# Optimization experiments

Measured on AMD Instinct MI355X. Metric: run time of the kernel, lower is better.

Reference implementation:

```python
import jax, jax.numpy as jnp
import numpy as np

B, S, M, D, H = 2, 2048, 512, 1024, 16
HD = D // H      # head dim 64
KVC = D // 16    # MLA kv compression dim 64
QC = D // 32     # MLA q compression dim 32
RD = HD          # retrieval (qk) head dim 64
LOOKBACK = 8     # cross_window
EPS = 1e-6


def rmsnorm(x, w):
    return x * jax.lax.rsqrt(jnp.mean(x * x, axis=-1, keepdims=True) + EPS) * w


def setup_inputs():
    key = jax.random.key(0)
    ks = jax.random.split(key, 20)
    g = lambda i, shape: jax.random.normal(ks[i], shape, jnp.float32) * 0.02
    return {
        "x": jax.random.normal(ks[0], (B, S, D), jnp.float32),
        "memory": jax.random.normal(ks[1], (B, M, D), jnp.float32),
        "seg_ids": jnp.sort(jax.random.randint(ks[2], (B, S), 0, M), axis=-1),
        "norm1_w": jnp.ones((D,), jnp.float32),
        "W_dq": g(3, (D, QC)),
        "W_uq": g(4, (QC, H * RD)),
        "W_dkv": g(5, (D, KVC)),
        "W_uk": g(6, (KVC, H * RD)),
        "W_uv": g(7, (KVC, H * HD)),
        "W_o_self": g(8, (H * HD, D)),
        "norm2_w": jnp.ones((D,), jnp.float32),
        "W_q_c": g(9, (D, D)),
        "W_k_c": g(10, (D, D)),
        "W_v_c": g(11, (D, D)),
        "W_o_c": g(12, (D, D)),
        "norm3_w": jnp.ones((D,), jnp.float32),
        "W_gate": g(13, (D, 4 * D)),
        "W_up": g(14, (D, 4 * D)),
        "W_down": g(15, (4 * D, D)),
    }


def reference(x, memory, seg_ids, norm1_w, W_dq, W_uq, W_dkv, W_uk, W_uv,
              W_o_self, norm2_w, W_q_c, W_k_c, W_v_c, W_o_c, norm3_w,
              W_gate, W_up, W_down):
    # ---- MLA causal self-attention (low-rank compressed q/kv) ----
    h = rmsnorm(x, norm1_w)
    q = ((h @ W_dq) @ W_uq).reshape(B, S, H, RD)
    c_kv = h @ W_dkv                                  # [B,S,KVC]
    k = (c_kv @ W_uk).reshape(B, S, H, RD)
    v = (c_kv @ W_uv).reshape(B, S, H, HD)
    scores = jnp.einsum('bihd,bjhd->bhij', q, k) / np.float32(np.sqrt(RD))
    causal = jnp.tril(jnp.ones((S, S), bool))
    scores = jnp.where(causal, scores, -jnp.inf)
    attn = jax.nn.softmax(scores, axis=-1)
    o = jnp.einsum('bhij,bjhd->bihd', attn, v).reshape(B, S, H * HD)
    x = x + o @ W_o_self
    # ---- segment sliding-window cross-attention ----
    h = rmsnorm(x, norm2_w)
    qc = (h @ W_q_c).reshape(B, S, H, HD)
    kc = (memory @ W_k_c).reshape(B, M, H, HD)
    vc = (memory @ W_v_c).reshape(B, M, H, HD)
    sc = jnp.einsum('bihd,bjhd->bhij', qc, kc) / np.float32(np.sqrt(HD))
    kv_pos = jnp.arange(M)
    seg = seg_ids[:, :, None]                          # [B,S,1]
    allowed = (kv_pos[None, None, :] <= seg) & (kv_pos[None, None, :] >= seg - LOOKBACK)
    sc = jnp.where(allowed[:, None, :, :], sc, -jnp.inf)
    ac = jax.nn.softmax(sc, axis=-1)
    oc = jnp.einsum('bhij,bjhd->bihd', ac, vc).reshape(B, S, D)
    x = x + oc @ W_o_c
    # ---- SwiGLU FFN ----
    h = rmsnorm(x, norm3_w)
    x = x + (jax.nn.silu(h @ W_gate) * (h @ W_up)) @ W_down
    return x
```

## Files before the change

### kernel.cpp

```cpp
#include <hip/hip_runtime.h>
#include <stdint.h>

typedef unsigned short U16;
typedef __bf16 bf16x8 __attribute__((ext_vector_type(8)));
typedef unsigned short us8 __attribute__((ext_vector_type(8)));
typedef float f32x4 __attribute__((ext_vector_type(4)));

__device__ __forceinline__ U16 f2bf(float f) {
    unsigned u = __builtin_bit_cast(unsigned, f);
    unsigned r = (u + 0x7fff + ((u >> 16) & 1)) >> 16;
    return (U16)r;
}
__device__ __forceinline__ U16 f2bf_fast(float f) {
    return (U16)((__builtin_bit_cast(unsigned, f) + 0x8000u) >> 16);
}
__device__ __forceinline__ float bf2f(U16 v) {
    return __builtin_bit_cast(float, (unsigned)v << 16);
}
__device__ __forceinline__ bf16x8 ld8(const U16* p) { return __builtin_bit_cast(bf16x8, *(const us8*)p); }

__device__ __forceinline__ void async16(const U16* g, U16* l) {
    auto* gp = (const __attribute__((address_space(1))) U16*)g;
    auto* lp = (__attribute__((address_space(3))) U16*)(uintptr_t)(uint32_t)(uintptr_t)l;
    __builtin_amdgcn_global_load_lds(gp, lp, 16, 0, 0);
}

struct WEnt { const float* src; U16* dst; int K, N, Kpad, Npad, koff, noff, tiles; };
struct WTable { WEnt e[13]; };

__global__ __launch_bounds__(256) void wtrans_all(WTable t) {
    int bx = blockIdx.x, ei = 0;
    while (bx >= t.e[ei].tiles) { bx -= t.e[ei].tiles; ei++; }
    const WEnt E = t.e[ei];
    const int ntn = E.Npad >> 5;
    const int n0 = (bx % ntn) * 32, k0 = (bx / ntn) * 32;
    __shared__ float tile[32][33];
    const int tx = threadIdx.x & 31, ty = threadIdx.x >> 5;
#pragma unroll
    for (int i = 0; i < 4; i++) {
        int kk = k0 + ty + i * 8, n = n0 + tx;
        int k = kk - E.koff;
        float v = (k >= 0 && k < E.K && n < E.N) ? E.src[(size_t)k * E.N + n] : 0.f;
        tile[ty + i * 8][tx] = v;
    }
    __syncthreads();
#pragma unroll
    for (int i = 0; i < 4; i++) {
        int n = n0 + ty + i * 8, kk = k0 + tx;
        E.dst[(size_t)(E.noff + n) * E.Kpad + kk] = f2bf(tile[tx][ty + i * 8]);
    }
}

__global__ __launch_bounds__(256) void f2bf_k(const float* __restrict__ in, U16* __restrict__ out, int n) {
    int i = (blockIdx.x * 256 + threadIdx.x) * 4;
    if (i < n) {
        float4 v = *(const float4*)(in + i);
        out[i + 0] = f2bf(v.x); out[i + 1] = f2bf(v.y);
        out[i + 2] = f2bf(v.z); out[i + 3] = f2bf(v.w);
    }
}

__global__ __launch_bounds__(256) void cq_reduce(const float* __restrict__ p, U16* __restrict__ out) {
    int i = (blockIdx.x * 256 + threadIdx.x) * 4;
    const float4 a = *(const float4*)(p + i);
    const float4 b = *(const float4*)(p + 524288 + i);
    const float4 c = *(const float4*)(p + 2 * 524288 + i);
    const float4 d = *(const float4*)(p + 3 * 524288 + i);
    out[i + 0] = f2bf(a.x + b.x + c.x + d.x);
    out[i + 1] = f2bf(a.y + b.y + c.y + d.y);
    out[i + 2] = f2bf(a.z + b.z + c.z + d.z);
    out[i + 3] = f2bf(a.w + b.w + c.w + d.w);
}

__global__ __launch_bounds__(256) void rmsnorm_k(const float* __restrict__ x, const float* __restrict__ w,
                                                 U16* __restrict__ h) {
    const int row = blockIdx.x, tid = threadIdx.x;
    const float4 v = *(const float4*)(x + (size_t)row * 1024 + tid * 4);
    float ss = v.x * v.x + v.y * v.y + v.z * v.z + v.w * v.w;
#pragma unroll
    for (int o = 32; o > 0; o >>= 1) ss += __shfl_xor(ss, o);
    __shared__ float red[4];
    if ((tid & 63) == 0) red[tid >> 6] = ss;
    __syncthreads();
    float tot = red[0] + red[1] + red[2] + red[3];
    float sc = rsqrtf(tot * (1.0f / 1024.0f) + 1e-6f);
    const float4 wv = *(const float4*)(w + tid * 4);
    U16* hp = h + (size_t)row * 1024 + tid * 4;
    hp[0] = f2bf(v.x * sc * wv.x); hp[1] = f2bf(v.y * sc * wv.y);
    hp[2] = f2bf(v.z * sc * wv.z); hp[3] = f2bf(v.w * sc * wv.w);
}

__global__ __launch_bounds__(256) void qkuv_gemm(const U16* __restrict__ A, const U16* __restrict__ Wuqk,
                                                 const U16* __restrict__ Wuv,
                                                 U16* __restrict__ qkb, U16* __restrict__ vt) {
    __shared__ __align__(16) U16 As[2][128 * 32];
    __shared__ __align__(16) U16 Bs[2][128 * 32];
    __shared__ __align__(16) U16 Ts[4][64 * 80];
    const int tid = threadIdx.x;
    const bool isuv = blockIdx.x >= 16;
    const U16* Bt = isuv ? Wuv : Wuqk;
    const int n0 = (isuv ? blockIdx.x - 16 : blockIdx.x) * 128;
    const int m0 = blockIdx.y * 128;
    const int wave = tid >> 6, lane = tid & 63, l16 = lane & 15, quad = lane >> 4;
    const int wm = (wave >> 1) * 64, wn = (wave & 1) * 64;
    const int sr = lane >> 2, sc = (lane & 3) * 8;
    const U16* gA = A + (size_t)(m0 + wave * 32 + sr) * 128 + sc;
    const U16* gB = Bt + (size_t)(n0 + wave * 32 + sr) * 128 + sc;
    f32x4 acc[4][4] = {};
    for (int kt = 0; kt < 128; kt += 64) {
        __syncthreads();
#pragma unroll
        for (int p = 0; p < 2; p++) {
            const int o = kt + p * 32;
            async16(gA + o, &As[p][(wave * 32) * 32]);
            async16(gA + 16 * 128 + o, &As[p][(wave * 32 + 16) * 32]);
            async16(gB + o, &Bs[p][(wave * 32) * 32]);
            async16(gB + 16 * 128 + o, &Bs[p][(wave * 32 + 16) * 32]);
        }
        __syncthreads();
#pragma unroll
        for (int p = 0; p < 2; p++) {
            bf16x8 af[4], bfr[4];
#pragma unroll
            for (int i = 0; i < 4; i++) {
                af[i]  = ld8(&As[p][(wm + i * 16 + l16) * 32 + quad * 8]);
                bfr[i] = ld8(&Bs[p][(wn + i * 16 + l16) * 32 + quad * 8]);
            }
#pragma unroll
            for (int mi = 0; mi < 4; mi++)
#pragma unroll
                for (int ni = 0; ni < 4; ni++)
                    acc[mi][ni] = __builtin_amdgcn_mfma_f32_16x16x32_bf16(af[mi], bfr[ni], acc[mi][ni], 0, 0, 0);
        }
    }
    if (isuv) {
        U16* T = Ts[wave];
#pragma unroll
        for (int mi = 0; mi < 4; mi++)
#pragma unroll
            for (int ni = 0; ni < 4; ni++)
#pragma unroll
                for (int r = 0; r < 4; r++)
                    T[(ni * 16 + l16) * 80 + mi * 16 + quad * 4 + r] = f2bf(acc[mi][ni][r]);
#pragma unroll
        for (int c = 0; c < 8; c++) {
            int nloc = (lane >> 3) + 8 * c, mloc = (lane & 7) * 8;
            us8 v = *(const us8*)&T[nloc * 80 + mloc];
            *(us8*)&vt[(size_t)(n0 + wn + nloc) * 4096 + (m0 + wm + mloc)] = v;
        }
    } else {
#pragma unroll
        for (int mi = 0; mi < 4; mi++)
#pragma unroll
            for (int r = 0; r < 4; r++) {
                int m = m0 + wm + mi * 16 + quad * 4 + r;
#pragma unroll
                for (int ni = 0; ni < 4; ni++)
                    qkb[(size_t)m * 2048 + n0 + wn + ni * 16 + l16] = f2bf(acc[mi][ni][r]);
            }
    }
}

template <int EPI>
__global__ __launch_bounds__(256) void gemm_m64(const U16* __restrict__ A, const U16* __restrict__ Bt,
                                                void* __restrict__ Cout, const float* __restrict__ resid,
                                                int M, int N, int K, int lda, int ldb, int ldc) {
    __shared__ __align__(16) U16 As[2][2][64 * 32];
    __shared__ __align__(16) U16 Bs[2][2][128 * 32];
    const int tid = threadIdx.x;
    const int m0 = blockIdx.y * 64, n0 = blockIdx.x * 128;
    const int k0 = blockIdx.z * K;
    const int wave = tid >> 6, lane = tid & 63, l16 = lane & 15, quad = lane >> 4;
    const int wm = (wave >> 1) * 32, wn = (wave & 1) * 64;
    const int sr = lane >> 2, sc = (lane & 3) * 8;
    const U16* gA = A + (size_t)(m0 + wave * 16 + sr) * lda + sc + k0;
    const U16* gB = Bt + (size_t)(n0 + wave * 32 + sr) * ldb + sc + k0;

    auto STAGE = [&](int buf, int kt) {
#pragma unroll
        for (int p = 0; p < 2; p++) {
            const int o = kt + p * 32;
            async16(gA + o, &As[buf][p][(wave * 16) * 32]);
            async16(gB + o, &Bs[buf][p][(wave * 32) * 32]);
            async16(gB + (size_t)16 * ldb + o, &Bs[buf][p][(wave * 32 + 16) * 32]);
        }
    };

    f32x4 acc[2][4] = {};
    const int NTK = K >> 6;
    STAGE(0, 0);
    STAGE(1, 64);
#pragma unroll 1
    for (int t = 0; t < NTK; ++t) {
        if (t == NTK - 1) asm volatile("s_waitcnt vmcnt(0)" ::: "memory");
        else              asm volatile("s_waitcnt vmcnt(6)" ::: "memory");
        __builtin_amdgcn_s_barrier();
        __builtin_amdgcn_sched_barrier(0);
        const int buf = t & 1;
#pragma unroll
        for (int p = 0; p < 2; p++) {
            bf16x8 af[2], bfr[4];
#pragma unroll
            for (int i = 0; i < 2; i++)
                af[i] = ld8(&As[buf][p][(wm + i * 16 + l16) * 32 + quad * 8]);
#pragma unroll
            for (int i = 0; i < 4; i++)
                bfr[i] = ld8(&Bs[buf][p][(wn + i * 16 + l16) * 32 + quad * 8]);
#pragma unroll
            for (int mi = 0; mi < 2; mi++)
#pragma unroll
                for (int ni = 0; ni < 4; ni++)
                    acc[mi][ni] = __builtin_amdgcn_mfma_f32_16x16x32_bf16(af[mi], bfr[ni], acc[mi][ni], 0, 0, 0);
        }
        __builtin_amdgcn_s_barrier();
        if (t + 2 < NTK) STAGE(buf, (t + 2) * 64);
    }
#pragma unroll
    for (int mi = 0; mi < 2; mi++) {
#pragma unroll
        for (int r = 0; r < 4; r++) {
            int m = m0 + wm + mi * 16 + quad * 4 + r;
#pragma unroll
            for (int ni = 0; ni < 4; ni++) {
                int n = n0 + wn + ni * 16 + l16;
                float val = acc[mi][ni][r];
                if (EPI == 0) ((U16*)Cout)[(size_t)m * ldc + n] = f2bf(val);
                else if (EPI == 1) ((float*)Cout)[(size_t)m * ldc + n] = resid[(size_t)m * ldc + n] + val;
                else if (EPI == 5) ((float*)Cout)[(size_t)blockIdx.z * 524288 + (size_t)m * ldc + n] = val;
            }
        }
    }
}

__global__ __launch_bounds__(256) void qckv_gemm(const U16* __restrict__ hbuf, const U16* __restrict__ Wqc,
                                                 const U16* __restrict__ memb, const U16* __restrict__ Wkvc,
                                                 U16* __restrict__ qcb, U16* __restrict__ kvcb) {
    __shared__ __align__(16) U16 As[2][2][64 * 32];
    __shared__ __align__(16) U16 Bs[2][2][128 * 32];
    const int tid = threadIdx.x, bid = blockIdx.x;
    const U16 *A, *Bt; U16* C; int m0, n0, ldc;
    if (bid < 512) { A = hbuf; Bt = Wqc;  C = qcb;  m0 = (bid >> 3) * 64; n0 = (bid & 7) * 128;  ldc = 1024; }
    else { int b2 = bid - 512; A = memb; Bt = Wkvc; C = kvcb; m0 = (b2 >> 4) * 64; n0 = (b2 & 15) * 128; ldc = 2048; }
    const int wave = tid >> 6, lane = tid & 63, l16 = lane & 15, quad = lane >> 4;
    const int wm = (wave >> 1) * 32, wn = (wave & 1) * 64;
    const int sr = lane >> 2, sc = (lane & 3) * 8;
    const U16* gA = A + (size_t)(m0 + wave * 16 + sr) * 1024 + sc;
    const U16* gB = Bt + (size_t)(n0 + wave * 32 + sr) * 1024 + sc;

    auto STAGE = [&](int buf, int kt) {
#pragma unroll
        for (int p = 0; p < 2; p++) {
            const int o = kt + p * 32;
            async16(gA + o, &As[buf][p][(wave * 16) * 32]);
            async16(gB + o, &Bs[buf][p][(wave * 32) * 32]);
            async16(gB + 16 * 1024 + o, &Bs[buf][p][(wave * 32 + 16) * 32]);
        }
    };

    f32x4 acc[2][4] = {};
    STAGE(0, 0);
    STAGE(1, 64);
#pragma unroll 1
    for (int t = 0; t < 16; ++t) {
        if (t == 15) asm volatile("s_waitcnt vmcnt(0)" ::: "memory");
        else         asm volatile("s_waitcnt vmcnt(6)" ::: "memory");
        __builtin_amdgcn_s_barrier();
        __builtin_amdgcn_sched_barrier(0);
        const int buf = t & 1;
#pragma unroll
        for (int p = 0; p < 2; p++) {
            bf16x8 af[2], bfr[4];
#pragma unroll
            for (int i = 0; i < 2; i++)
                af[i] = ld8(&As[buf][p][(wm + i * 16 + l16) * 32 + quad * 8]);
#pragma unroll
            for (int i = 0; i < 4; i++)
                bfr[i] = ld8(&Bs[buf][p][(wn + i * 16 + l16) * 32 + quad * 8]);
#pragma unroll
            for (int mi = 0; mi < 2; mi++)
#pragma unroll
                for (int ni = 0; ni < 4; ni++)
                    acc[mi][ni] = __builtin_amdgcn_mfma_f32_16x16x32_bf16(af[mi], bfr[ni], acc[mi][ni], 0, 0, 0);
        }
        __builtin_amdgcn_s_barrier();
        if (t + 2 < 16) STAGE(buf, (t + 2) * 64);
    }
#pragma unroll
    for (int mi = 0; mi < 2; mi++)
#pragma unroll
        for (int r = 0; r < 4; r++) {
            int m = m0 + wm + mi * 16 + quad * 4 + r;
#pragma unroll
            for (int ni = 0; ni < 4; ni++)
                C[(size_t)m * ldc + n0 + wn + ni * 16 + l16] = f2bf(acc[mi][ni][r]);
        }
}

__global__ __launch_bounds__(512, 2) void ffn1_8ph(const U16* __restrict__ A, const U16* __restrict__ Wgu,
                                                   U16* __restrict__ Cout) {
    __shared__ __align__(16) U16 As[2][256 * 64];
    __shared__ __align__(16) U16 Bs[2][256 * 64];
    const int tid = threadIdx.x;
    const int wid = tid >> 6, lane = tid & 63;
    const int l16 = lane & 15, quad = lane >> 4;
    const int n0 = blockIdx.x * 128;
    const int m0 = blockIdx.y * 256;
    const int wr = wid >> 2, wc = wid & 3;
    const int wm = wr * 128;
    const int wn = wc * 64;
    const int srow = lane >> 3;
    const int schunk = (lane & 7) ^ srow;
    const U16* gA = A + (size_t)(m0 + wid * 32 + srow) * 1024 + schunk * 8;
    const U16* gB = Wgu + (size_t)((wid & 1) * 4096 + n0 + (wid >> 1) * 32 + srow) * 1024 + schunk * 8;

    auto STAGE = [&](int buf, int kt) {
        U16* la = &As[buf][(wid * 32) * 64];
        U16* lb = &Bs[buf][(wid * 32) * 64];
        const U16* pa = gA + kt;
        const U16* pb = gB + kt;
#pragma unroll
        for (int j = 0; j < 4; ++j) {
            async16(pa + j * 8 * 1024, la + j * 8 * 64);
            async16(pb + j * 8 * 1024, lb + j * 8 * 64);
        }
    };

    f32x4 acc[8][4] = {};

    auto TILE = [&](int buf) {
        const U16* Ab = &As[buf][0];
        const U16* Bb = &Bs[buf][0];
        const int cx = l16 & 7;
        bf16x8 a0[4][2], a1[4][2], b0[2][2], b1[2][2];
#pragma unroll
        for (int mi = 0; mi < 4; ++mi)
#pragma unroll
            for (int kh = 0; kh < 2; ++kh)
                a0[mi][kh] = ld8(&Ab[(wm + mi * 16 + l16) * 64 + (((kh * 4 + quad) ^ cx) << 3)]);
#pragma unroll
        for (int ni = 0; ni < 2; ++ni)
#pragma unroll
            for (int kh = 0; kh < 2; ++kh)
                b0[ni][kh] = ld8(&Bb[(wn + ni * 16 + l16) * 64 + (((kh * 4 + quad) ^ cx) << 3)]);
#pragma unroll
        for (int ni = 0; ni < 2; ++ni)
#pragma unroll
            for (int kh = 0; kh < 2; ++kh)
                b1[ni][kh] = ld8(&Bb[(wn + 32 + ni * 16 + l16) * 64 + (((kh * 4 + quad) ^ cx) << 3)]);
        __builtin_amdgcn_s_setprio(1);
#pragma unroll
        for (int mi = 0; mi < 4; ++mi)
#pragma unroll
            for (int ni = 0; ni < 2; ++ni)
#pragma unroll
                for (int kh = 0; kh < 2; ++kh)
                    acc[mi][ni] = __builtin_amdgcn_mfma_f32_16x16x32_bf16(a0[mi][kh], b0[ni][kh], acc[mi][ni], 0, 0, 0);
        __builtin_amdgcn_s_setprio(0);
#pragma unroll
        for (int mi = 0; mi < 4; ++mi)
#pragma unroll
            for (int kh = 0; kh < 2; ++kh)
                a1[mi][kh] = ld8(&Ab[(wm + 64 + mi * 16 + l16) * 64 + (((kh * 4 + quad) ^ cx) << 3)]);
        __builtin_amdgcn_s_setprio(1);
#pragma unroll
        for (int mi = 0; mi < 4; ++mi)
#pragma unroll
            for (int ni = 0; ni < 2; ++ni)
#pragma unroll
                for (int kh = 0; kh < 2; ++kh)
                    acc[mi][2 + ni] = __builtin_amdgcn_mfma_f32_16x16x32_bf16(a0[mi][kh], b1[ni][kh], acc[mi][2 + ni], 0, 0, 0);
        __builtin_amdgcn_s_setprio(0);
        __builtin_amdgcn_s_setprio(1);
#pragma unroll
        for (int mi = 0; mi < 4; ++mi)
#pragma unroll
            for (int ni = 0; ni < 2; ++ni)
#pragma unroll
                for (int kh = 0; kh < 2; ++kh)
                    acc[4 + mi][2 + ni] = __builtin_amdgcn_mfma_f32_16x16x32_bf16(a1[mi][kh], b1[ni][kh], acc[4 + mi][2 + ni], 0, 0, 0);
        __builtin_amdgcn_s_setprio(0);
        __builtin_amdgcn_s_setprio(1);
#pragma unroll
        for (int mi = 0; mi < 4; ++mi)
#pragma unroll
            for (int ni = 0; ni < 2; ++ni)
#pragma unroll
                for (int kh = 0; kh < 2; ++kh)
                    acc[4 + mi][ni] = __builtin_amdgcn_mfma_f32_16x16x32_bf16(a1[mi][kh], b0[ni][kh], acc[4 + mi][ni], 0, 0, 0);
        __builtin_amdgcn_s_setprio(0);
    };

    STAGE(0, 0);
    STAGE(1, 64);
#pragma unroll 1
    for (int t2 = 0; t2 < 7; ++t2) {
        asm volatile("s_waitcnt vmcnt(8)" ::: "memory");
        __builtin_amdgcn_s_barrier();
        __builtin_amdgcn_sched_barrier(0);
        TILE(0);
        __builtin_amdgcn_s_barrier();
        STAGE(0, (2 * t2 + 2) * 64);
        asm volatile("s_waitcnt vmcnt(8)" ::: "memory");
        __builtin_amdgcn_s_barrier();
        __builtin_amdgcn_sched_barrier(0);
        TILE(1);
        __builtin_amdgcn_s_barrier();
        STAGE(1, (2 * t2 + 3) * 64);
    }
    asm volatile("s_waitcnt vmcnt(8)" ::: "memory");
    __builtin_amdgcn_s_barrier();
    __builtin_amdgcn_sched_barrier(0);
    TILE(0);
    asm volatile("s_waitcnt vmcnt(0)" ::: "memory");
    __builtin_amdgcn_s_barrier();
    __builtin_amdgcn_sched_barrier(0);
    TILE(1);

#pragma unroll
    for (int mi = 0; mi < 8; ++mi)
#pragma unroll
        for (int r = 0; r < 4; ++r) {
            int m = m0 + wm + mi * 16 + quad * 4 + r;
#pragma unroll
            for (int ni = 0; ni < 2; ++ni) {
                int col = n0 + wc * 32 + ni * 16 + l16;
                float g = acc[mi][ni][r], u = acc[mi][ni + 2][r];
                float act = g / (1.f + __expf(-g)) * u;
                Cout[(size_t)m * 4096 + col] = f2bf(act);
            }
        }
}

__global__ __launch_bounds__(256, 3) void flash_self4(const U16* __restrict__ QK, const U16* __restrict__ Vt,
                                                      U16* __restrict__ Og) {
    __shared__ __align__(16) U16 Ks[2][32 * 64];
    __shared__ __align__(16) U16 Vs[2][64 * 32];
    __shared__ __align__(16) U16 Ps[4][1280];
    const int wave = threadIdx.x >> 6, lane = threadIdx.x & 63;
    const int l16 = lane & 15, quad = lane >> 4;
    const int bx = blockIdx.x;
    const int T = 15 - (bx >> 5);
    const int bh = bx & 31, b = bh >> 4, h = bh & 15;
    const int q0 = T * 128;
    const int NT = 4 * T + 4;
    const int G0 = q0 + wave * 16, G1 = q0 + 64 + wave * 16;
    bf16x8 aq[2][2];
    {
        const size_t r0 = (size_t)(b * 2048 + G0 + l16) * 2048 + h * 64;
        const size_t r1 = (size_t)(b * 2048 + G1 + l16) * 2048 + h * 64;
        aq[0][0] = ld8(QK + r0 + quad * 8); aq[0][1] = ld8(QK + r0 + 32 + quad * 8);
        aq[1][0] = ld8(QK + r1 + quad * 8); aq[1][1] = ld8(QK + r1 + 32 + quad * 8);
    }
    const int krow = wave * 8 + (lane >> 3);
    const int kchunk = (lane & 7) ^ (lane >> 3);
    const U16* gK = QK + (size_t)(b * 2048 + krow) * 2048 + 1024 + h * 64 + kchunk * 8;
    const int vrow = wave * 16 + (lane >> 2);
    const int vchunk = (lane & 3) ^ ((lane >> 2) & 3) ^ ((lane >> 4) & 3);
    const U16* gV = Vt + (size_t)(h * 64 + vrow) * 4096 + b * 2048 + vchunk * 8;

    auto STAGE = [&](int buf, int j0) {
        async16(gK + (size_t)j0 * 2048, &Ks[buf][(wave * 8) * 64]);
        async16(gV + j0, &Vs[buf][(wave * 16) * 32]);
    };

    f32x4 o[2][4] = {};
    float ls[2][4] = {};
    U16* Pw = Ps[wave];
    const int prd = l16 * 40 + ((quad ^ (l16 >> 2)) << 3);

    auto TILE = [&](int buf, int j0) {
        bf16x8 kf[2][2];
#pragma unroll
        for (int jh = 0; jh < 2; ++jh)
#pragma unroll
            for (int kh = 0; kh < 2; ++kh)
                kf[jh][kh] = ld8(&Ks[buf][(jh * 16 + l16) * 64 + (((kh * 4 + quad) ^ (l16 & 7)) << 3)]);
        bf16x8 vf[4];
#pragma unroll
        for (int dg = 0; dg < 4; ++dg)
            vf[dg] = ld8(&Vs[buf][(dg * 16 + l16) * 32 + ((quad ^ (l16 & 3) ^ ((l16 >> 2) & 3)) << 3)]);
#pragma unroll
        for (int g = 0; g < 2; ++g) {
            const int G = g ? G1 : G0;
            if (j0 < G + 16) {
                f32x4 s0 = {}, s1 = {};
                __builtin_amdgcn_s_setprio(1);
                s0 = __builtin_amdgcn_mfma_f32_16x16x32_bf16(aq[g][0], kf[0][0], s0, 0, 0, 0);
                s0 = __builtin_amdgcn_mfma_f32_16x16x32_bf16(aq[g][1], kf[0][1], s0, 0, 0, 0);
                s1 = __builtin_amdgcn_mfma_f32_16x16x32_bf16(aq[g][0], kf[1][0], s1, 0, 0, 0);
                s1 = __builtin_amdgcn_mfma_f32_16x16x32_bf16(aq[g][1], kf[1][1], s1, 0, 0, 0);
                __builtin_amdgcn_s_setprio(0);
                float p0[4], p1[4];
                if (j0 + 32 > G) {
#pragma unroll
                    for (int r = 0; r < 4; ++r) {
                        int qg = G + quad * 4 + r;
                        p0[r] = (j0 + l16 <= qg) ? __expf(fminf(s0[r] * 0.125f, 30.f)) : 0.f;
                        p1[r] = (j0 + 16 + l16 <= qg) ? __expf(fminf(s1[r] * 0.125f, 30.f)) : 0.f;
                    }
                } else {
#pragma unroll
                    for (int r = 0; r < 4; ++r) {
                        p0[r] = __expf(fminf(s0[r] * 0.125f, 30.f));
                        p1[r] = __expf(fminf(s1[r] * 0.125f, 30.f));
                    }
                }
#pragma unroll
                for (int r = 0; r < 4; ++r) {
                    ls[g][r] += p0[r] + p1[r];
                    int row = quad * 4 + r;
                    Pw[g * 640 + row * 40 + ((((l16 >> 3) + 0) ^ quad) << 3) + (l16 & 7)] = f2bf_fast(p0[r]);
                    Pw[g * 640 + row * 40 + ((((l16 >> 3) + 2) ^ quad) << 3) + (l16 & 7)] = f2bf_fast(p1[r]);
                }
                bf16x8 ap = ld8(&Pw[g * 640 + prd]);
                __builtin_amdgcn_s_setprio(1);
                o[g][0] = __builtin_amdgcn_mfma_f32_16x16x32_bf16(ap, vf[0], o[g][0], 0, 0, 0);
                o[g][1] = __builtin_amdgcn_mfma_f32_16x16x32_bf16(ap, vf[1], o[g][1], 0, 0, 0);
                o[g][2] = __builtin_amdgcn_mfma_f32_16x16x32_bf16(ap, vf[2], o[g][2], 0, 0, 0);
                o[g][3] = __builtin_amdgcn_mfma_f32_16x16x32_bf16(ap, vf[3], o[g][3], 0, 0, 0);
                __builtin_amdgcn_s_setprio(0);
            }
        }
    };

    STAGE(0, 0);
    STAGE(1, 32);
#pragma unroll 1
    for (int it = 0; it < NT - 2; ++it) {
        asm volatile("s_waitcnt vmcnt(2)" ::: "memory");
        __builtin_amdgcn_s_barrier();
        __builtin_amdgcn_sched_barrier(0);
        TILE(it & 1, it * 32);
        __builtin_amdgcn_s_barrier();
        STAGE(it & 1, (it + 2) * 32);
    }
    asm volatile("s_waitcnt vmcnt(2)" ::: "memory");
    __builtin_amdgcn_s_barrier();
    __builtin_amdgcn_sched_barrier(0);
    TILE(NT & 1, (NT - 2) * 32);
    asm volatile("s_waitcnt vmcnt(0)" ::: "memory");
    __builtin_amdgcn_s_barrier();
    __builtin_amdgcn_sched_barrier(0);
    TILE((NT - 1) & 1, (NT - 1) * 32);

#pragma unroll
    for (int g = 0; g < 2; ++g) {
        const int G = g ? G1 : G0;
#pragma unroll
        for (int r = 0; r < 4; ++r) {
            float v = ls[g][r];
            v += __shfl_xor(v, 1); v += __shfl_xor(v, 2);
            v += __shfl_xor(v, 4); v += __shfl_xor(v, 8);
            float inv = 1.0f / v;
            int qrow = G + quad * 4 + r;
            U16* op = Og + (size_t)(b * 2048 + qrow) * 1024 + h * 64 + l16;
#pragma unroll
            for (int dg = 0; dg < 4; ++dg)
                op[dg * 16] = f2bf(o[g][dg][r] * inv);
        }
    }
}

__global__ __launch_bounds__(256) void cross_attn(const U16* __restrict__ qc, const U16* __restrict__ kvc,
                                                  const int* __restrict__ seg_ids, U16* __restrict__ oc) {
    const int tok = blockIdx.x;
    const int b = tok >> 11;
    const int w = threadIdx.x >> 6, lane = threadIdx.x & 63;
    const int h = blockIdx.y * 4 + w;
    const int seg = seg_ids[tok];
    const size_t qoff = (size_t)tok * 1024 + h * 64 + lane;
    float q = bf2f(qc[qoff]);
    float s[9];
#pragma unroll
    for (int jj = 0; jj < 9; jj++) {
        int j = seg - 8 + jj;
        float sc = -INFINITY;
        if (j >= 0) {
            float kv = bf2f(kvc[((size_t)(b * 512) + j) * 2048 + h * 64 + lane]);
            sc = q * kv;
            sc += __shfl_xor(sc, 1); sc += __shfl_xor(sc, 2); sc += __shfl_xor(sc, 4);
            sc += __shfl_xor(sc, 8); sc += __shfl_xor(sc, 16); sc += __shfl_xor(sc, 32);
            sc *= 0.125f;
        }
        s[jj] = sc;
    }
    float m = s[0];
#pragma unroll
    for (int jj = 1; jj < 9; jj++) m = fmaxf(m, s[jj]);
    float l = 0.f, o = 0.f;
#pragma unroll
    for (int jj = 0; jj < 9; jj++) {
        int j = seg - 8 + jj;
        if (j >= 0) {
            float p = __expf(s[jj] - m);
            l += p;
            o += p * bf2f(kvc[((size_t)(b * 512) + j) * 2048 + 1024 + h * 64 + lane]);
        }
    }
    oc[qoff] = f2bf(o / l);
}

extern "C" void kernel_launch(void* const* d_in, const int* in_sizes, int n_in,
                              void* d_out, int out_size, void* d_ws, size_t ws_size,
                              hipStream_t stream) {
    const float* x      = (const float*)d_in[0];
    const float* memory = (const float*)d_in[1];
    const int*   seg    = (const int*)d_in[2];
    const float* n1w    = (const float*)d_in[3];
    const float* W_dq   = (const float*)d_in[4];
    const float* W_uq   = (const float*)d_in[5];
    const float* W_dkv  = (const float*)d_in[6];
    const float* W_uk   = (const float*)d_in[7];
    const float* W_uv   = (const float*)d_in[8];
    const float* W_os   = (const float*)d_in[9];
    const float* n2w    = (const float*)d_in[10];
    const float* W_qc   = (const float*)d_in[11];
    const float* W_kc   = (const float*)d_in[12];
    const float* W_vc   = (const float*)d_in[13];
    const float* W_oc   = (const float*)d_in[14];
    const float* n3w    = (const float*)d_in[15];
    const float* W_gate = (const float*)d_in[16];
    const float* W_up   = (const float*)d_in[17];
    const float* W_down = (const float*)d_in[18];
    (void)in_sizes; (void)n_in; (void)out_size; (void)ws_size;

    char* ws = (char*)d_ws;
    size_t off = 0;
    auto alloc = [&](size_t bytes) -> void* {
        void* p = ws + off;
        off += (bytes + 255) & ~(size_t)255;
        return p;
    };
    const size_t MB = 1024 * 1024;
    U16* hbuf     = (U16*)alloc(8 * MB);
    float* x1     = (float*)alloc(16 * MB);
    float* x2     = (float*)alloc(16 * MB);
    float* cq32   = (float*)alloc(8 * MB);
    U16* Wt_dqkv  = (U16*)alloc(128 * 1024 * 2);
    U16* Wt_uqk   = (U16*)alloc(2048 * 128 * 2);
    U16* Wt_uv    = (U16*)alloc(1024 * 128 * 2);
    U16* Wt_os    = (U16*)alloc(1024 * 1024 * 2);
    U16* Wt_qc    = (U16*)alloc(1024 * 1024 * 2);
    U16* Wt_kvc   = (U16*)alloc((size_t)2048 * 1024 * 2);
    U16* Wt_oc    = (U16*)alloc(1024 * 1024 * 2);
    U16* Wt_gu    = (U16*)alloc((size_t)8192 * 1024 * 2);
    U16* Wt_down  = (U16*)alloc((size_t)1024 * 4096 * 2);
    U16* mem_bf   = (U16*)alloc(1024 * 1024 * 2);
    char* arena   = ws + off;
    U16* cq  = (U16*)(arena);
    U16* qkb = (U16*)(arena + 1 * MB);
    U16* vt  = (U16*)(arena + 17 * MB);
    U16* ob  = (U16*)(arena + 25 * MB);
    U16* qcb  = (U16*)(arena);
    U16* kvcb = (U16*)(arena + 8 * MB);
    U16* ocb  = (U16*)(arena + 12 * MB);
    U16* gact = (U16*)(arena);

    WTable T;
    int i = 0;
    auto ent = [&](const float* s, U16* d, int K, int N, int Kpad, int Npad, int koff, int noff) {
        T.e[i++] = WEnt{s, d, K, N, Kpad, Npad, koff, noff, (Kpad >> 5) * (Npad >> 5)};
    };
    ent(W_dq,   Wt_dqkv, 1024, 32,   1024, 32,   0,  0);
    ent(W_dkv,  Wt_dqkv, 1024, 64,   1024, 96,   0,  32);
    ent(W_uq,   Wt_uqk,  32,   1024, 128,  1024, 0,  0);
    ent(W_uk,   Wt_uqk,  64,   1024, 128,  1024, 32, 1024);
    ent(W_uv,   Wt_uv,   64,   1024, 128,  1024, 32, 0);
    ent(W_os,   Wt_os,   1024, 1024, 1024, 1024, 0,  0);
    ent(W_qc,   Wt_qc,   1024, 1024, 1024, 1024, 0,  0);
    ent(W_kc,   Wt_kvc,  1024, 1024, 1024, 1024, 0,  0);
    ent(W_vc,   Wt_kvc,  1024, 1024, 1024, 1024, 0,  1024);
    ent(W_oc,   Wt_oc,   1024, 1024, 1024, 1024, 0,  0);
    ent(W_gate, Wt_gu,   1024, 4096, 1024, 4096, 0,  0);
    ent(W_up,   Wt_gu,   1024, 4096, 1024, 4096, 0,  4096);
    ent(W_down, Wt_down, 4096, 1024, 4096, 1024, 0,  0);
    int total_tiles = 0;
    for (int j = 0; j < 13; j++) total_tiles += T.e[j].tiles;
    wtrans_all<<<total_tiles, 256, 0, stream>>>(T);
    f2bf_k<<<1024, 256, 0, stream>>>(memory, mem_bf, 1024 * 1024);

    rmsnorm_k<<<4096, 256, 0, stream>>>(x, n1w, hbuf);
    gemm_m64<5><<<dim3(1, 64, 4), 256, 0, stream>>>(hbuf, Wt_dqkv, cq32, nullptr, 4096, 128, 256, 1024, 1024, 128);
    cq_reduce<<<512, 256, 0, stream>>>(cq32, cq);
    qkuv_gemm<<<dim3(24, 32), 256, 0, stream>>>(cq, Wt_uqk, Wt_uv, qkb, vt);
    flash_self4<<<512, 256, 0, stream>>>(qkb, vt, ob);
    gemm_m64<1><<<dim3(8, 64), 256, 0, stream>>>(ob, Wt_os, x1, x, 4096, 1024, 1024, 1024, 1024, 1024);

    rmsnorm_k<<<4096, 256, 0, stream>>>(x1, n2w, hbuf);
    qckv_gemm<<<768, 256, 0, stream>>>(hbuf, Wt_qc, mem_bf, Wt_kvc, qcb, kvcb);
    cross_attn<<<dim3(4096, 4), 256, 0, stream>>>(qcb, kvcb, seg, ocb);
    gemm_m64<1><<<dim3(8, 64), 256, 0, stream>>>(ocb, Wt_oc, x2, x1, 4096, 1024, 1024, 1024, 1024, 1024);

    rmsnorm_k<<<4096, 256, 0, stream>>>(x2, n3w, hbuf);
    ffn1_8ph<<<dim3(32, 16), 512, 0, stream>>>(hbuf, Wt_gu, gact);
    gemm_m64<1><<<dim3(8, 64), 256, 0, stream>>>(gact, Wt_down, (float*)d_out, x2, 4096, 1024, 4096, 4096, 4096, 1024);
}
```

Before: 499.6 us.

## Enlarge GEMM tiles to 128x128 with XOR-swizzled 64-wide LDS layout

Replaces the 64x128 GEMM tile kernels (gemm_m64 and qckv_gemm) with 128x128 tiles using a single 64-wide K panel stored in LDS with an XOR chunk swizzle, and raises MFMA priority with s_setprio around the compute block. Each wave now computes a 64x64 sub-tile, which doubles register accumulators and raises arithmetic intensity per LDS load. The aim is fewer global loads per flop and fewer LDS bank conflicts. In exchange, grids shrink (e.g. 256 blocks for 1024-wide outputs on a 256-CU part), which can reduce occupancy and wave-level parallelism.

```diff
diff --git a/kernel.cpp b/kernel.cpp
--- a/kernel.cpp
+++ b/kernel.cpp
@@ -162,66 +162,70 @@
 }
 
 template <int EPI>
-__global__ __launch_bounds__(256) void gemm_m64(const U16* __restrict__ A, const U16* __restrict__ Bt,
-                                                void* __restrict__ Cout, const float* __restrict__ resid,
-                                                int M, int N, int K, int lda, int ldb, int ldc) {
-    __shared__ __align__(16) U16 As[2][2][64 * 32];
-    __shared__ __align__(16) U16 Bs[2][2][128 * 32];
+__global__ __launch_bounds__(256) void gemm_m128(const U16* __restrict__ A, const U16* __restrict__ Bt,
+                                                 void* __restrict__ Cout, const float* __restrict__ resid,
+                                                 int M, int N, int K, int lda, int ldb, int ldc) {
+    __shared__ __align__(16) U16 As[2][128 * 64];
+    __shared__ __align__(16) U16 Bs[2][128 * 64];
     const int tid = threadIdx.x;
-    const int m0 = blockIdx.y * 64, n0 = blockIdx.x * 128;
+    const int m0 = blockIdx.y * 128, n0 = blockIdx.x * 128;
     const int k0 = blockIdx.z * K;
     const int wave = tid >> 6, lane = tid & 63, l16 = lane & 15, quad = lane >> 4;
-    const int wm = (wave >> 1) * 32, wn = (wave & 1) * 64;
-    const int sr = lane >> 2, sc = (lane & 3) * 8;
-    const U16* gA = A + (size_t)(m0 + wave * 16 + sr) * lda + sc + k0;
-    const U16* gB = Bt + (size_t)(n0 + wave * 32 + sr) * ldb + sc + k0;
+    const int wm = (wave >> 1) * 64, wn = (wave & 1) * 64;
+    const int srow = lane >> 3;
+    const int schunk = (lane & 7) ^ srow;
+    const U16* gA = A + (size_t)(m0 + wave * 32 + srow) * lda + schunk * 8 + k0;
+    const U16* gB = Bt + (size_t)(n0 + wave * 32 + srow) * ldb + schunk * 8 + k0;
 
     auto STAGE = [&](int buf, int kt) {
-#pragma unroll
-        for (int p = 0; p < 2; p++) {
-            const int o = kt + p * 32;
-            async16(gA + o, &As[buf][p][(wave * 16) * 32]);
-            async16(gB + o, &Bs[buf][p][(wave * 32) * 32]);
-            async16(gB + (size_t)16 * ldb + o, &Bs[buf][p][(wave * 32 + 16) * 32]);
+        U16* la = &As[buf][(wave * 32) * 64];
+        U16* lb = &Bs[buf][(wave * 32) * 64];
+#pragma unroll
+        for (int j = 0; j < 4; ++j) {
+            async16(gA + kt + (size_t)j * 8 * lda, la + j * 8 * 64);
+            async16(gB + kt + (size_t)j * 8 * ldb, lb + j * 8 * 64);
         }
     };
 
-    f32x4 acc[2][4] = {};
+    f32x4 acc[4][4] = {};
     const int NTK = K >> 6;
     STAGE(0, 0);
     STAGE(1, 64);
 #pragma unroll 1
     for (int t = 0; t < NTK; ++t) {
         if (t == NTK - 1) asm volatile("s_waitcnt vmcnt(0)" ::: "memory");
-        else              asm volatile("s_waitcnt vmcnt(6)" ::: "memory");
+        else              asm volatile("s_waitcnt vmcnt(8)" ::: "memory");
         __builtin_amdgcn_s_barrier();
         __builtin_amdgcn_sched_barrier(0);
         const int buf = t & 1;
-#pragma unroll
-        for (int p = 0; p < 2; p++) {
-            bf16x8 af[2], bfr[4];
-#pragma unroll
-            for (int i = 0; i < 2; i++)
-                af[i] = ld8(&As[buf][p][(wm + i * 16 + l16) * 32 + quad * 8]);
-#pragma unroll
-            for (int i = 0; i < 4; i++)
-                bfr[i] = ld8(&Bs[buf][p][(wn + i * 16 + l16) * 32 + quad * 8]);
-#pragma unroll
-            for (int mi = 0; mi < 2; mi++)
-#pragma unroll
-                for (int ni = 0; ni < 4; ni++)
-                    acc[mi][ni] = __builtin_amdgcn_mfma_f32_16x16x32_bf16(af[mi], bfr[ni], acc[mi][ni], 0, 0, 0);
-        }
+        const int cx = l16 & 7;
+        bf16x8 af[4][2], bfr[4][2];
+#pragma unroll
+        for (int i = 0; i < 4; ++i)
+#pragma unroll
+            for (int kh = 0; kh < 2; ++kh) {
+                af[i][kh]  = ld8(&As[buf][(wm + i * 16 + l16) * 64 + (((kh * 4 + quad) ^ cx) << 3)]);
+                bfr[i][kh] = ld8(&Bs[buf][(wn + i * 16 + l16) * 64 + (((kh * 4 + quad) ^ cx) << 3)]);
+            }
+        __builtin_amdgcn_s_setprio(1);
+#pragma unroll
+        for (int mi = 0; mi < 4; ++mi)
+#pragma unroll
+            for (int ni = 0; ni < 4; ++ni)
+#pragma unroll
+                for (int kh = 0; kh < 2; ++kh)
+                    acc[mi][ni] = __builtin_amdgcn_mfma_f32_16x16x32_bf16(af[mi][kh], bfr[ni][kh], acc[mi][ni], 0, 0, 0);
+        __builtin_amdgcn_s_setprio(0);
         __builtin_amdgcn_s_barrier();
         if (t + 2 < NTK) STAGE(buf, (t + 2) * 64);
     }
 #pragma unroll
-    for (int mi = 0; mi < 2; mi++) {
-#pragma unroll
-        for (int r = 0; r < 4; r++) {
+    for (int mi = 0; mi < 4; ++mi) {
+#pragma unroll
+        for (int r = 0; r < 4; ++r) {
             int m = m0 + wm + mi * 16 + quad * 4 + r;
 #pragma unroll
-            for (int ni = 0; ni < 4; ni++) {
+            for (int ni = 0; ni < 4; ++ni) {
                 int n = n0 + wn + ni * 16 + l16;
                 float val = acc[mi][ni][r];
                 if (EPI == 0) ((U16*)Cout)[(size_t)m * ldc + n] = f2bf(val);
@@ -235,63 +239,67 @@
 __global__ __launch_bounds__(256) void qckv_gemm(const U16* __restrict__ hbuf, const U16* __restrict__ Wqc,
                                                  const U16* __restrict__ memb, const U16* __restrict__ Wkvc,
                                                  U16* __restrict__ qcb, U16* __restrict__ kvcb) {
-    __shared__ __align__(16) U16 As[2][2][64 * 32];
-    __shared__ __align__(16) U16 Bs[2][2][128 * 32];
+    __shared__ __align__(16) U16 As[2][128 * 64];
+    __shared__ __align__(16) U16 Bs[2][128 * 64];
     const int tid = threadIdx.x, bid = blockIdx.x;
     const U16 *A, *Bt; U16* C; int m0, n0, ldc;
-    if (bid < 512) { A = hbuf; Bt = Wqc;  C = qcb;  m0 = (bid >> 3) * 64; n0 = (bid & 7) * 128;  ldc = 1024; }
-    else { int b2 = bid - 512; A = memb; Bt = Wkvc; C = kvcb; m0 = (b2 >> 4) * 64; n0 = (b2 & 15) * 128; ldc = 2048; }
+    if (bid < 256) { A = hbuf; Bt = Wqc;  C = qcb;  m0 = (bid >> 3) * 128; n0 = (bid & 7) * 128;  ldc = 1024; }
+    else { int b2 = bid - 256; A = memb; Bt = Wkvc; C = kvcb; m0 = (b2 >> 4) * 128; n0 = (b2 & 15) * 128; ldc = 2048; }
     const int wave = tid >> 6, lane = tid & 63, l16 = lane & 15, quad = lane >> 4;
-    const int wm = (wave >> 1) * 32, wn = (wave & 1) * 64;
-    const int sr = lane >> 2, sc = (lane & 3) * 8;
-    const U16* gA = A + (size_t)(m0 + wave * 16 + sr) * 1024 + sc;
-    const U16* gB = Bt + (size_t)(n0 + wave * 32 + sr) * 1024 + sc;
+    const int wm = (wave >> 1) * 64, wn = (wave & 1) * 64;
+    const int srow = lane >> 3;
+    const int schunk = (lane & 7) ^ srow;
+    const U16* gA = A + (size_t)(m0 + wave * 32 + srow) * 1024 + schunk * 8;
+    const U16* gB = Bt + (size_t)(n0 + wave * 32 + srow) * 1024 + schunk * 8;
 
     auto STAGE = [&](int buf, int kt) {
-#pragma unroll
-        for (int p = 0; p < 2; p++) {
-            const int o = kt + p * 32;
-            async16(gA + o, &As[buf][p][(wave * 16) * 32]);
-            async16(gB + o, &Bs[buf][p][(wave * 32) * 32]);
-            async16(gB + 16 * 1024 + o, &Bs[buf][p][(wave * 32 + 16) * 32]);
+        U16* la = &As[buf][(wave * 32) * 64];
+        U16* lb = &Bs[buf][(wave * 32) * 64];
+#pragma unroll
+        for (int j = 0; j < 4; ++j) {
+            async16(gA + kt + (size_t)j * 8 * 1024, la + j * 8 * 64);
+            async16(gB + kt + (size_t)j * 8 * 1024, lb + j * 8 * 64);
         }
     };
 
-    f32x4 acc[2][4] = {};
+    f32x4 acc[4][4] = {};
     STAGE(0, 0);
     STAGE(1, 64);
 #pragma unroll 1
     for (int t = 0; t < 16; ++t) {
         if (t == 15) asm volatile("s_waitcnt vmcnt(0)" ::: "memory");
-        else         asm volatile("s_waitcnt vmcnt(6)" ::: "memory");
+        else         asm volatile("s_waitcnt vmcnt(8)" ::: "memory");
         __builtin_amdgcn_s_barrier();
         __builtin_amdgcn_sched_barrier(0);
         const int buf = t & 1;
-#pragma unroll
-        for (int p = 0; p < 2; p++) {
-            bf16x8 af[2], bfr[4];
-#pragma unroll
-            for (int i = 0; i < 2; i++)
-                af[i] = ld8(&As[buf][p][(wm + i * 16 + l16) * 32 + quad * 8]);
-#pragma unroll
-            for (int i = 0; i < 4; i++)
-                bfr[i] = ld8(&Bs[buf][p][(wn + i * 16 + l16) * 32 + quad * 8]);
-#pragma unroll
-            for (int mi = 0; mi < 2; mi++)
-#pragma unroll
-                for (int ni = 0; ni < 4; ni++)
-                    acc[mi][ni] = __builtin_amdgcn_mfma_f32_16x16x32_bf16(af[mi], bfr[ni], acc[mi][ni], 0, 0, 0);
-        }
+        const int cx = l16 & 7;
+        bf16x8 af[4][2], bfr[4][2];
+#pragma unroll
+        for (int i = 0; i < 4; ++i)
+#pragma unroll
+            for (int kh = 0; kh < 2; ++kh) {
+                af[i][kh]  = ld8(&As[buf][(wm + i * 16 + l16) * 64 + (((kh * 4 + quad) ^ cx) << 3)]);
+                bfr[i][kh] = ld8(&Bs[buf][(wn + i * 16 + l16) * 64 + (((kh * 4 + quad) ^ cx) << 3)]);
+            }
+        __builtin_amdgcn_s_setprio(1);
+#pragma unroll
+        for (int mi = 0; mi < 4; ++mi)
+#pragma unroll
+            for (int ni = 0; ni < 4; ++ni)
+#pragma unroll
+                for (int kh = 0; kh < 2; ++kh)
+                    acc[mi][ni] = __builtin_amdgcn_mfma_f32_16x16x32_bf16(af[mi][kh], bfr[ni][kh], acc[mi][ni], 0, 0, 0);
+        __builtin_amdgcn_s_setprio(0);
         __builtin_amdgcn_s_barrier();
         if (t + 2 < 16) STAGE(buf, (t + 2) * 64);
     }
 #pragma unroll
-    for (int mi = 0; mi < 2; mi++)
-#pragma unroll
-        for (int r = 0; r < 4; r++) {
+    for (int mi = 0; mi < 4; ++mi)
+#pragma unroll
+        for (int r = 0; r < 4; ++r) {
             int m = m0 + wm + mi * 16 + quad * 4 + r;
 #pragma unroll
-            for (int ni = 0; ni < 4; ni++)
+            for (int ni = 0; ni < 4; ++ni)
                 C[(size_t)m * ldc + n0 + wn + ni * 16 + l16] = f2bf(acc[mi][ni][r]);
         }
 }
@@ -680,18 +688,18 @@
     f2bf_k<<<1024, 256, 0, stream>>>(memory, mem_bf, 1024 * 1024);
 
     rmsnorm_k<<<4096, 256, 0, stream>>>(x, n1w, hbuf);
-    gemm_m64<5><<<dim3(1, 64, 4), 256, 0, stream>>>(hbuf, Wt_dqkv, cq32, nullptr, 4096, 128, 256, 1024, 1024, 128);
+    gemm_m128<5><<<dim3(1, 32, 4), 256, 0, stream>>>(hbuf, Wt_dqkv, cq32, nullptr, 4096, 128, 256, 1024, 1024, 128);
     cq_reduce<<<512, 256, 0, stream>>>(cq32, cq);
     qkuv_gemm<<<dim3(24, 32), 256, 0, stream>>>(cq, Wt_uqk, Wt_uv, qkb, vt);
     flash_self4<<<512, 256, 0, stream>>>(qkb, vt, ob);
-    gemm_m64<1><<<dim3(8, 64), 256, 0, stream>>>(ob, Wt_os, x1, x, 4096, 1024, 1024, 1024, 1024, 1024);
+    gemm_m128<1><<<dim3(8, 32), 256, 0, stream>>>(ob, Wt_os, x1, x, 4096, 1024, 1024, 1024, 1024, 1024);
 
     rmsnorm_k<<<4096, 256, 0, stream>>>(x1, n2w, hbuf);
-    qckv_gemm<<<768, 256, 0, stream>>>(hbuf, Wt_qc, mem_bf, Wt_kvc, qcb, kvcb);
+    qckv_gemm<<<384, 256, 0, stream>>>(hbuf, Wt_qc, mem_bf, Wt_kvc, qcb, kvcb);
     cross_attn<<<dim3(4096, 4), 256, 0, stream>>>(qcb, kvcb, seg, ocb);
-    gemm_m64<1><<<dim3(8, 64), 256, 0, stream>>>(ocb, Wt_oc, x2, x1, 4096, 1024, 1024, 1024, 1024, 1024);
+    gemm_m128<1><<<dim3(8, 32), 256, 0, stream>>>(ocb, Wt_oc, x2, x1, 4096, 1024, 1024, 1024, 1024, 1024);
 
     rmsnorm_k<<<4096, 256, 0, stream>>>(x2, n3w, hbuf);
     ffn1_8ph<<<dim3(32, 16), 512, 0, stream>>>(hbuf, Wt_gu, gact);
-    gemm_m64<1><<<dim3(8, 64), 256, 0, stream>>>(gact, Wt_down, (float*)d_out, x2, 4096, 1024, 4096, 4096, 4096, 1024);
-}
+    gemm_m128<1><<<dim3(8, 32), 256, 0, stream>>>(gact, Wt_down, (float*)d_out, x2, 4096, 1024, 4096, 4096, 4096, 1024);
+}
```

Measured after the change: 489.1 us. -2.1%, faster.
